# Kernel tuning notes

Measured on AMD Instinct MI355X. Metric: run time of the kernel, lower is better.

The kernel has to match this reference:

```python
import jax, jax.numpy as jnp
import numpy as np

N, D, N_CLASSES = 8192, 512, 128
POS_MARGIN = 1.0  # default path: sample_method=None, Dynamic_margin=None


def setup_inputs() -> dict:
    key = jax.random.key(0)
    k1, k2 = jax.random.split(key)
    x = jax.random.normal(k1, (N, D), dtype=jnp.float32)
    # metric-learning embeddings are L2-normalized so sim in [-1, 1]
    x = x / jnp.linalg.norm(x, axis=1, keepdims=True)
    targets = jax.random.randint(k2, (N,), 0, N_CLASSES, dtype=jnp.int64)
    return {"inputs": x, "targets": targets, "nonorm": 0}


def reference(inputs, targets, nonorm):
    n = inputs.shape[0]
    sim = jnp.matmul(inputs, inputs.T)                      # [n, n]
    same = targets[:, None] == targets[None, :]             # [n, n]
    pos_mask = same & (sim < POS_MARGIN)                    # drops self-sim == 1
    neg_mask = ~same

    # per-row masked log-sum-exp (sort in original is irrelevant to the sums)
    pos_sum = jnp.sum(jnp.where(pos_mask, jnp.exp(1.0 - sim), 0.0), axis=1)
    neg_sum = jnp.sum(jnp.where(neg_mask, jnp.exp(sim), 0.0), axis=1)
    pos_loss = jnp.log(pos_sum)
    neg_loss = jnp.log(neg_sum)

    has_neg = jnp.any(neg_mask, axis=1)                     # rows w/o negs are skipped
    loss = jnp.sum(jnp.where(has_neg, pos_loss + neg_loss, 0.0)) / n
    prec = jnp.mean(1.0 - has_neg.astype(jnp.float32))      # fraction of skipped rows

    # torch code reports means of the LAST row's pos/neg pairs
    last_pos = pos_mask[-1]
    last_neg = neg_mask[-1]
    mean_pos_sim = jnp.sum(jnp.where(last_pos, sim[-1], 0.0)) / jnp.sum(last_pos)
    mean_neg_sim = jnp.sum(jnp.where(last_neg, sim[-1], 0.0)) / jnp.sum(last_neg)
    return loss, prec, mean_pos_sim, mean_neg_sim
```

## Files before the change

kernel.cpp:

```cpp
#include <hip/hip_runtime.h>
#include <math.h>

#define N_ 8192
#define D_ 512
#define NC_ 128
#define T_ 64

typedef __attribute__((ext_vector_type(8))) short bf16x8;
typedef __attribute__((ext_vector_type(4))) float f32x4;
typedef __attribute__((ext_vector_type(4))) unsigned short us4;

static __device__ __forceinline__ unsigned short f2bf(float f) {
    union { float f; unsigned u; } c; c.f = f;
    unsigned u = c.u;
    u += 0x7fffu + ((u >> 16) & 1u);
    return (unsigned short)(u >> 16);
}

__global__ __launch_bounds__(256) void k_convert(const float* __restrict__ x,
                                                 unsigned short* __restrict__ xb) {
    int i = (blockIdx.x * 256 + threadIdx.x);
    float4 v = reinterpret_cast<const float4*>(x)[i];
    us4 o = { f2bf(v.x), f2bf(v.y), f2bf(v.z), f2bf(v.w) };
    reinterpret_cast<us4*>(xb)[i] = o;
}

__global__ __launch_bounds__(256, 4) void k_main(const unsigned short* __restrict__ xb,
                                                 const int* __restrict__ tg,
                                                 float* __restrict__ bufP,
                                                 float* __restrict__ bufN) {
    __shared__ alignas(16) unsigned short As[128 * 64];
    __shared__ alignas(16) unsigned short Bs[128 * 64];
    __shared__ int rowT[128];

    const int tid  = threadIdx.x;
    const int w    = tid >> 6;
    const int lane = tid & 63;
    const int q    = lane >> 4;
    const int l15  = lane & 15;
    const int wrow = w >> 1;
    const int wcol = w & 1;

    int rem = blockIdx.x;
    int it = 0;
    while (rem >= (T_ - it)) { rem -= (T_ - it); it++; }
    const int jt = it + rem;
    const int row0 = it * 128;
    const int col0 = jt * 128;

    if (tid < 128) rowT[tid] = tg[row0 + tid];
    __syncthreads();

    int tR[4][4];
#pragma unroll
    for (int mi = 0; mi < 4; ++mi)
#pragma unroll
        for (int r = 0; r < 4; ++r)
            tR[mi][r] = rowT[wrow * 64 + mi * 16 + q * 4 + r];

    int tC[4];
#pragma unroll
    for (int ni = 0; ni < 4; ++ni)
        tC[ni] = tg[col0 + wcol * 64 + ni * 16 + l15];

    f32x4 acc[4][4];
#pragma unroll
    for (int mi = 0; mi < 4; ++mi)
#pragma unroll
        for (int ni = 0; ni < 4; ++ni)
            acc[mi][ni] = (f32x4){0.f, 0.f, 0.f, 0.f};

    for (int ks = 0; ks < 8; ++ks) {
        const int k0 = ks * 64;
        __syncthreads();
#pragma unroll
        for (int itr = 0; itr < 4; ++itr) {
            int gs = (itr * 4 + w) * 64 + lane;
            int r  = gs >> 3;
            int s  = gs & 7;
            int g  = s ^ (r & 7);
            const unsigned short* ga = xb + (size_t)(row0 + r) * D_ + k0 + g * 8;
            const unsigned short* gb = xb + (size_t)(col0 + r) * D_ + k0 + g * 8;
            __builtin_amdgcn_global_load_lds(
                (const __attribute__((address_space(1))) void*)ga,
                (__attribute__((address_space(3))) void*)(As + (itr * 4 + w) * 512),
                16, 0, 0);
            __builtin_amdgcn_global_load_lds(
                (const __attribute__((address_space(1))) void*)gb,
                (__attribute__((address_space(3))) void*)(Bs + (itr * 4 + w) * 512),
                16, 0, 0);
        }
        __syncthreads();

#pragma unroll
        for (int kc = 0; kc < 2; ++kc) {
            bf16x8 aF[4], bF[4];
#pragma unroll
            for (int mi = 0; mi < 4; ++mi) {
                int rA = wrow * 64 + mi * 16 + l15;
                int g  = kc * 4 + q;
                int s  = g ^ (rA & 7);
                aF[mi] = *reinterpret_cast<const bf16x8*>(As + rA * 64 + s * 8);
            }
#pragma unroll
            for (int ni = 0; ni < 4; ++ni) {
                int rB = wcol * 64 + ni * 16 + l15;
                int g  = kc * 4 + q;
                int s  = g ^ (rB & 7);
                bF[ni] = *reinterpret_cast<const bf16x8*>(Bs + rB * 64 + s * 8);
            }
#pragma unroll
            for (int mi = 0; mi < 4; ++mi)
#pragma unroll
                for (int ni = 0; ni < 4; ++ni)
                    acc[mi][ni] = __builtin_amdgcn_mfma_f32_16x16x32_bf16(
                        aF[mi], bF[ni], acc[mi][ni], 0, 0, 0);
        }
    }

    float ps[4][4], ns[4][4];
    float cps[4], cns[4];
#pragma unroll
    for (int mi = 0; mi < 4; ++mi)
#pragma unroll
        for (int r = 0; r < 4; ++r) { ps[mi][r] = 0.f; ns[mi][r] = 0.f; }
#pragma unroll
    for (int ni = 0; ni < 4; ++ni) { cps[ni] = 0.f; cns[ni] = 0.f; }

#pragma unroll
    for (int mi = 0; mi < 4; ++mi)
#pragma unroll
        for (int ni = 0; ni < 4; ++ni)
#pragma unroll
            for (int r = 0; r < 4; ++r) {
                float s = acc[mi][ni][r];
                bool same = (tR[mi][r] == tC[ni]);
                float e = __expf(same ? 1.0f - s : s);
                float pe = (same && (s < 1.0f)) ? e : 0.0f;
                float ne = same ? 0.0f : e;
                ps[mi][r] += pe; ns[mi][r] += ne;
                cps[ni]   += pe; cns[ni]   += ne;
            }

    __syncthreads();
    float* scr = (float*)As;

#pragma unroll
    for (int mi = 0; mi < 4; ++mi)
#pragma unroll
        for (int r = 0; r < 4; ++r) {
            float p = ps[mi][r];
            float n = ns[mi][r];
#pragma unroll
            for (int m = 1; m < 16; m <<= 1) {
                p += __shfl_xor(p, m, 64);
                n += __shfl_xor(n, m, 64);
            }
            if (l15 == 0) {
                int rloc = wrow * 64 + mi * 16 + q * 4 + r;
                scr[wcol * 128 + rloc]       = p;
                scr[256 + wcol * 128 + rloc] = n;
            }
        }

#pragma unroll
    for (int ni = 0; ni < 4; ++ni) {
        float p = cps[ni];
        float n = cns[ni];
        p += __shfl_xor(p, 16, 64); p += __shfl_xor(p, 32, 64);
        n += __shfl_xor(n, 16, 64); n += __shfl_xor(n, 32, 64);
        if (q == 0) {
            int cloc = wcol * 64 + ni * 16 + l15;
            scr[512 + wrow * 128 + cloc] = p;
            scr[768 + wrow * 128 + cloc] = n;
        }
    }
    __syncthreads();

    if (tid < 128) {
        int r = tid;
        size_t off = ((size_t)it * T_ + jt) * 128 + r;
        bufP[off] = scr[r]       + scr[128 + r];
        bufN[off] = scr[256 + r] + scr[384 + r];
    } else if (jt != it) {
        int c = tid - 128;
        size_t off = ((size_t)jt * T_ + it) * 128 + c;
        bufP[off] = scr[512 + c] + scr[640 + c];
        bufN[off] = scr[768 + c] + scr[896 + c];
    }
}

__global__ __launch_bounds__(256) void k_last(const float* __restrict__ x,
                                              double* __restrict__ sim_last) {
    int j    = (blockIdx.x * 256 + threadIdx.x) >> 6;
    int lane = threadIdx.x & 63;
    const float* xl = x + (size_t)(N_ - 1) * D_;
    const float* xj = x + (size_t)j * D_;
    double acc = 0.0;
#pragma unroll
    for (int it = 0; it < 8; ++it) {
        int k = it * 64 + lane;
        acc += (double)xl[k] * (double)xj[k];
    }
#pragma unroll
    for (int m = 32; m >= 1; m >>= 1) acc += __shfl_xor(acc, m, 64);
    if (lane == 0) sim_last[j] = acc;
}

__global__ __launch_bounds__(256) void k_reduce(const float* __restrict__ bufP,
                                                const float* __restrict__ bufN,
                                                float* __restrict__ psum,
                                                float* __restrict__ nsum) {
    int t    = blockIdx.x;
    int half = threadIdx.x >> 7;
    int r    = threadIdx.x & 127;
    const float* buf = half ? bufN : bufP;
    const float* base = buf + (size_t)t * T_ * 128 + r;
    float s = 0.f;
#pragma unroll
    for (int o = 0; o < T_; ++o) s += base[o * 128];
    if (half) nsum[t * 128 + r] = s;
    else      psum[t * 128 + r] = s;
}

__global__ __launch_bounds__(1024) void k_final(const float* __restrict__ psum,
                                                const float* __restrict__ nsum,
                                                const int* __restrict__ tg,
                                                const double* __restrict__ sim_last,
                                                float* __restrict__ out) {
    __shared__ int lh[NC_];
    __shared__ double sl[1024], sp[1024], sn[1024];
    __shared__ int    sk[1024], cp[1024], cn[1024];
    int tid = threadIdx.x;

    if (tid < NC_) lh[tid] = 0;
    __syncthreads();
    for (int i = tid; i < N_; i += 1024) atomicAdd(&lh[tg[i]], 1);
    __syncthreads();

    double part = 0.0;
    int skip = 0;
    for (int i = tid; i < N_; i += 1024) {
        if (lh[tg[i]] < N_) {
            part += (double)(logf(psum[i]) + logf(nsum[i]));
        } else {
            skip++;
        }
    }

    double pd = 0.0, nd = 0.0;
    int pc = 0, nc = 0;
    int tlast = tg[N_ - 1];
    for (int j = tid; j < N_; j += 1024) {
        double s = sim_last[j];
        if (tg[j] == tlast) {
            if (s < 1.0) { pd += s; pc++; }
        } else {
            nd += s; nc++;
        }
    }

    sl[tid] = part; sk[tid] = skip;
    sp[tid] = pd;   cp[tid] = pc;
    sn[tid] = nd;   cn[tid] = nc;
    __syncthreads();
    for (int s = 512; s >= 1; s >>= 1) {
        if (tid < s) {
            sl[tid] += sl[tid + s]; sk[tid] += sk[tid + s];
            sp[tid] += sp[tid + s]; cp[tid] += cp[tid + s];
            sn[tid] += sn[tid + s]; cn[tid] += cn[tid + s];
        }
        __syncthreads();
    }
    if (tid == 0) {
        out[0] = (float)(sl[0] / (double)N_);
        out[1] = (float)sk[0] / (float)N_;
        out[2] = (float)(sp[0] / (double)cp[0]);
        out[3] = (float)(sn[0] / (double)cn[0]);
    }
}

extern "C" void kernel_launch(void* const* d_in, const int* in_sizes, int n_in,
                              void* d_out, int out_size, void* d_ws, size_t ws_size,
                              hipStream_t stream) {
    const float* x  = (const float*)d_in[0];
    const int*   tg = (const int*)d_in[1];
    char* ws = (char*)d_ws;

    unsigned short* xb = (unsigned short*)ws;
    const size_t XB = (size_t)N_ * D_ * 2;
    float*  psum     = (float*)(ws + XB);
    float*  nsum     = (float*)(ws + XB + 32768);
    double* sim_last = (double*)(ws + XB + 65536);
    float*  bufP     = (float*)(ws + XB + 131072);
    float*  bufN     = (float*)(ws + XB + 131072 + 2097152);

    const int nblk_tri = T_ * (T_ + 1) / 2;

    hipLaunchKernelGGL(k_convert, dim3((N_ * D_) / (256 * 4)), dim3(256), 0, stream, x, xb);
    hipLaunchKernelGGL(k_main, dim3(nblk_tri), dim3(256), 0, stream, xb, tg, bufP, bufN);
    hipLaunchKernelGGL(k_last, dim3((N_ * 64) / 256), dim3(256), 0, stream, x, sim_last);
    hipLaunchKernelGGL(k_reduce, dim3(T_), dim3(256), 0, stream, bufP, bufN, psum, nsum);
    hipLaunchKernelGGL(k_final, dim3(1), dim3(1024), 0, stream,
                       psum, nsum, tg, sim_last, (float*)d_out);
}
```

Before: 165.3 us.

## Double-buffer GEMM LDS tiles, swizzle block order, and fuse post-processing kernels

The main similarity kernel now uses two LDS buffers and issues asynchronous global-to-LDS loads two K-steps ahead, with explicit waitcnt and barriers. This overlaps memory latency with MFMA work, and setprio raises priority during the MFMA burst. Block indices are swizzled across the triangular tile grid, and occupancy is lowered to 2 blocks per CU to fit the doubled shared memory. The separate last-row, reduce and final kernels are merged into one 64-block post kernel that finishes through global atomics and a last-block-done counter, cutting launches and removing the single-block tail, at the cost of atomic ordering subtleties.

```diff
diff --git a/kernel.cpp b/kernel.cpp
--- a/kernel.cpp
+++ b/kernel.cpp
@@ -5,6 +5,8 @@
 #define D_ 512
 #define NC_ 128
 #define T_ 64
+#define BK_ 64
+#define KSTEPS 8
 
 typedef __attribute__((ext_vector_type(8))) short bf16x8;
 typedef __attribute__((ext_vector_type(4))) float f32x4;
@@ -17,21 +19,31 @@
     return (unsigned short)(u >> 16);
 }
 
-__global__ __launch_bounds__(256) void k_convert(const float* __restrict__ x,
-                                                 unsigned short* __restrict__ xb) {
-    int i = (blockIdx.x * 256 + threadIdx.x);
+__global__ __launch_bounds__(256) void k_pre(const float* __restrict__ x,
+                                             unsigned short* __restrict__ xb,
+                                             double* __restrict__ gd,
+                                             int* __restrict__ gi) {
+    const int bid = blockIdx.x;
+    const int tid = threadIdx.x;
+    if (bid == 0 && tid == 0) {
+        atomicExch((unsigned long long*)&gd[0], 0ull);
+        atomicExch((unsigned long long*)&gd[1], 0ull);
+        atomicExch((unsigned long long*)&gd[2], 0ull);
+        atomicExch(&gi[0], 0); atomicExch(&gi[1], 0);
+        atomicExch(&gi[2], 0); atomicExch(&gi[3], 0);
+    }
+    int i = bid * 256 + tid;
     float4 v = reinterpret_cast<const float4*>(x)[i];
     us4 o = { f2bf(v.x), f2bf(v.y), f2bf(v.z), f2bf(v.w) };
     reinterpret_cast<us4*>(xb)[i] = o;
 }
 
-__global__ __launch_bounds__(256, 4) void k_main(const unsigned short* __restrict__ xb,
+__global__ __launch_bounds__(256, 2) void k_main(const unsigned short* __restrict__ xb,
                                                  const int* __restrict__ tg,
                                                  float* __restrict__ bufP,
                                                  float* __restrict__ bufN) {
-    __shared__ alignas(16) unsigned short As[128 * 64];
-    __shared__ alignas(16) unsigned short Bs[128 * 64];
-    __shared__ int rowT[128];
+    __shared__ alignas(16) unsigned short As[2][128 * 64];
+    __shared__ alignas(16) unsigned short Bs[2][128 * 64];
 
     const int tid  = threadIdx.x;
     const int w    = tid >> 6;
@@ -41,38 +53,17 @@
     const int wrow = w >> 1;
     const int wcol = w & 1;
 
-    int rem = blockIdx.x;
+    const int bswz = (blockIdx.x & 7) * 260 + (blockIdx.x >> 3);
+
+    int rem = bswz;
     int it = 0;
     while (rem >= (T_ - it)) { rem -= (T_ - it); it++; }
     const int jt = it + rem;
     const int row0 = it * 128;
     const int col0 = jt * 128;
 
-    if (tid < 128) rowT[tid] = tg[row0 + tid];
-    __syncthreads();
-
-    int tR[4][4];
-#pragma unroll
-    for (int mi = 0; mi < 4; ++mi)
-#pragma unroll
-        for (int r = 0; r < 4; ++r)
-            tR[mi][r] = rowT[wrow * 64 + mi * 16 + q * 4 + r];
-
-    int tC[4];
-#pragma unroll
-    for (int ni = 0; ni < 4; ++ni)
-        tC[ni] = tg[col0 + wcol * 64 + ni * 16 + l15];
-
-    f32x4 acc[4][4];
-#pragma unroll
-    for (int mi = 0; mi < 4; ++mi)
-#pragma unroll
-        for (int ni = 0; ni < 4; ++ni)
-            acc[mi][ni] = (f32x4){0.f, 0.f, 0.f, 0.f};
-
-    for (int ks = 0; ks < 8; ++ks) {
-        const int k0 = ks * 64;
-        __syncthreads();
+    auto stage_tile = [&](int p, int kt) {
+        const int k0 = kt * BK_;
 #pragma unroll
         for (int itr = 0; itr < 4; ++itr) {
             int gs = (itr * 4 + w) * 64 + lane;
@@ -83,47 +74,90 @@
             const unsigned short* gb = xb + (size_t)(col0 + r) * D_ + k0 + g * 8;
             __builtin_amdgcn_global_load_lds(
                 (const __attribute__((address_space(1))) void*)ga,
-                (__attribute__((address_space(3))) void*)(As + (itr * 4 + w) * 512),
+                (__attribute__((address_space(3))) void*)(&As[p][0] + (itr * 4 + w) * 512),
                 16, 0, 0);
             __builtin_amdgcn_global_load_lds(
                 (const __attribute__((address_space(1))) void*)gb,
-                (__attribute__((address_space(3))) void*)(Bs + (itr * 4 + w) * 512),
+                (__attribute__((address_space(3))) void*)(&Bs[p][0] + (itr * 4 + w) * 512),
                 16, 0, 0);
         }
-        __syncthreads();
-
+    };
+
+    f32x4 acc[4][4];
+#pragma unroll
+    for (int mi = 0; mi < 4; ++mi)
+#pragma unroll
+        for (int ni = 0; ni < 4; ++ni)
+            acc[mi][ni] = (f32x4){0.f, 0.f, 0.f, 0.f};
+
+    auto compute_tile = [&](int p) {
 #pragma unroll
         for (int kc = 0; kc < 2; ++kc) {
             bf16x8 aF[4], bF[4];
 #pragma unroll
             for (int mi = 0; mi < 4; ++mi) {
                 int rA = wrow * 64 + mi * 16 + l15;
-                int g  = kc * 4 + q;
-                int s  = g ^ (rA & 7);
-                aF[mi] = *reinterpret_cast<const bf16x8*>(As + rA * 64 + s * 8);
+                int sl = (kc * 4 + q) ^ (rA & 7);
+                aF[mi] = *reinterpret_cast<const bf16x8*>(&As[p][0] + rA * 64 + sl * 8);
             }
 #pragma unroll
             for (int ni = 0; ni < 4; ++ni) {
                 int rB = wcol * 64 + ni * 16 + l15;
-                int g  = kc * 4 + q;
-                int s  = g ^ (rB & 7);
-                bF[ni] = *reinterpret_cast<const bf16x8*>(Bs + rB * 64 + s * 8);
-            }
+                int sl = (kc * 4 + q) ^ (rB & 7);
+                bF[ni] = *reinterpret_cast<const bf16x8*>(&Bs[p][0] + rB * 64 + sl * 8);
+            }
+            asm volatile("s_waitcnt lgkmcnt(0)" ::: "memory");
+            __builtin_amdgcn_sched_barrier(0);
+            __builtin_amdgcn_s_setprio(1);
 #pragma unroll
             for (int mi = 0; mi < 4; ++mi)
 #pragma unroll
                 for (int ni = 0; ni < 4; ++ni)
                     acc[mi][ni] = __builtin_amdgcn_mfma_f32_16x16x32_bf16(
                         aF[mi], bF[ni], acc[mi][ni], 0, 0, 0);
-        }
-    }
+            __builtin_amdgcn_s_setprio(0);
+        }
+    };
+
+#define TILE(P, KS, DOSTAGE, VMN)                                         \
+    do {                                                                  \
+        asm volatile("s_waitcnt vmcnt(" #VMN ")" ::: "memory");           \
+        __builtin_amdgcn_s_barrier();                                     \
+        __builtin_amdgcn_sched_barrier(0);                                \
+        compute_tile(P);                                                  \
+        __builtin_amdgcn_s_barrier();                                     \
+        __builtin_amdgcn_sched_barrier(0);                                \
+        if (DOSTAGE) stage_tile(P, (KS) + 2);                             \
+    } while (0)
+
+    stage_tile(0, 0);
+    stage_tile(1, 1);
+
+    TILE(0, 0, 1, 8);
+    TILE(1, 1, 1, 8);
+    TILE(0, 2, 1, 8);
+    TILE(1, 3, 1, 8);
+    TILE(0, 4, 1, 8);
+    TILE(1, 5, 1, 8);
+    TILE(0, 6, 0, 8);
+    TILE(1, 7, 0, 0);
+#undef TILE
+
+    int tC[4];
+#pragma unroll
+    for (int ni = 0; ni < 4; ++ni)
+        tC[ni] = tg[col0 + wcol * 64 + ni * 16 + l15];
 
     float ps[4][4], ns[4][4];
     float cps[4], cns[4];
+    int tR[4][4];
 #pragma unroll
     for (int mi = 0; mi < 4; ++mi)
 #pragma unroll
-        for (int r = 0; r < 4; ++r) { ps[mi][r] = 0.f; ns[mi][r] = 0.f; }
+        for (int r = 0; r < 4; ++r) {
+            ps[mi][r] = 0.f; ns[mi][r] = 0.f;
+            tR[mi][r] = tg[row0 + wrow * 64 + mi * 16 + q * 4 + r];
+        }
 #pragma unroll
     for (int ni = 0; ni < 4; ++ni) { cps[ni] = 0.f; cns[ni] = 0.f; }
 
@@ -142,9 +176,7 @@
                 cps[ni]   += pe; cns[ni]   += ne;
             }
 
-    __syncthreads();
     float* scr = (float*)As;
-
 #pragma unroll
     for (int mi = 0; mi < 4; ++mi)
 #pragma unroll
@@ -190,93 +222,101 @@
     }
 }
 
-__global__ __launch_bounds__(256) void k_last(const float* __restrict__ x,
-                                              double* __restrict__ sim_last) {
-    int j    = (blockIdx.x * 256 + threadIdx.x) >> 6;
-    int lane = threadIdx.x & 63;
-    const float* xl = x + (size_t)(N_ - 1) * D_;
-    const float* xj = x + (size_t)j * D_;
-    double acc = 0.0;
-#pragma unroll
-    for (int it = 0; it < 8; ++it) {
-        int k = it * 64 + lane;
-        acc += (double)xl[k] * (double)xj[k];
-    }
-#pragma unroll
-    for (int m = 32; m >= 1; m >>= 1) acc += __shfl_xor(acc, m, 64);
-    if (lane == 0) sim_last[j] = acc;
-}
-
-__global__ __launch_bounds__(256) void k_reduce(const float* __restrict__ bufP,
-                                                const float* __restrict__ bufN,
-                                                float* __restrict__ psum,
-                                                float* __restrict__ nsum) {
-    int t    = blockIdx.x;
-    int half = threadIdx.x >> 7;
-    int r    = threadIdx.x & 127;
-    const float* buf = half ? bufN : bufP;
+__global__ __launch_bounds__(256) void k_post(const float* __restrict__ bufP,
+                                              const float* __restrict__ bufN,
+                                              const int* __restrict__ tg,
+                                              const float* __restrict__ x,
+                                              double* __restrict__ gd,
+                                              int* __restrict__ gi,
+                                              float* __restrict__ out) {
+    __shared__ int lh[NC_];
+    __shared__ float sv[256];
+    __shared__ double Rd[256], Pd[256], Nd[256];
+    __shared__ int Ri[256], Pc[256], Nc[256];
+    const int t   = blockIdx.x;
+    const int tid = threadIdx.x;
+
+    if (tid < NC_) lh[tid] = 0;
+    __syncthreads();
+#pragma unroll
+    for (int i = 0; i < 32; ++i) atomicAdd(&lh[tg[i * 256 + tid]], 1);
+    __syncthreads();
+
+    const int half = tid >> 7;
+    const int r    = tid & 127;
+    const float* buf  = half ? bufN : bufP;
     const float* base = buf + (size_t)t * T_ * 128 + r;
     float s = 0.f;
 #pragma unroll
     for (int o = 0; o < T_; ++o) s += base[o * 128];
-    if (half) nsum[t * 128 + r] = s;
-    else      psum[t * 128 + r] = s;
-}
-
-__global__ __launch_bounds__(1024) void k_final(const float* __restrict__ psum,
-                                                const float* __restrict__ nsum,
-                                                const int* __restrict__ tg,
-                                                const double* __restrict__ sim_last,
-                                                float* __restrict__ out) {
-    __shared__ int lh[NC_];
-    __shared__ double sl[1024], sp[1024], sn[1024];
-    __shared__ int    sk[1024], cp[1024], cn[1024];
-    int tid = threadIdx.x;
-
-    if (tid < NC_) lh[tid] = 0;
-    __syncthreads();
-    for (int i = tid; i < N_; i += 1024) atomicAdd(&lh[tg[i]], 1);
-    __syncthreads();
-
-    double part = 0.0;
-    int skip = 0;
-    for (int i = tid; i < N_; i += 1024) {
-        if (lh[tg[i]] < N_) {
-            part += (double)(logf(psum[i]) + logf(nsum[i]));
-        } else {
-            skip++;
-        }
-    }
-
+    sv[tid] = s;
+    __syncthreads();
+
+    double rd = 0.0; int ri = 0;
+    if (tid < 128) {
+        int row = t * 128 + tid;
+        bool ok = lh[tg[row]] < N_;
+        rd = ok ? (double)(logf(sv[tid]) + logf(sv[128 + tid])) : 0.0;
+        ri = ok ? 0 : 1;
+    }
+
+    const int wv   = tid >> 6;
+    const int lane = tid & 63;
+    const int tlast = tg[N_ - 1];
+    const float* xl = x + (size_t)(N_ - 1) * D_;
     double pd = 0.0, nd = 0.0;
     int pc = 0, nc = 0;
-    int tlast = tg[N_ - 1];
-    for (int j = tid; j < N_; j += 1024) {
-        double s = sim_last[j];
-        if (tg[j] == tlast) {
-            if (s < 1.0) { pd += s; pc++; }
-        } else {
-            nd += s; nc++;
-        }
-    }
-
-    sl[tid] = part; sk[tid] = skip;
-    sp[tid] = pd;   cp[tid] = pc;
-    sn[tid] = nd;   cn[tid] = nc;
-    __syncthreads();
-    for (int s = 512; s >= 1; s >>= 1) {
-        if (tid < s) {
-            sl[tid] += sl[tid + s]; sk[tid] += sk[tid + s];
-            sp[tid] += sp[tid + s]; cp[tid] += cp[tid + s];
-            sn[tid] += sn[tid + s]; cn[tid] += cn[tid + s];
+    for (int rep = 0; rep < 32; ++rep) {
+        int row = t * 128 + rep * 4 + wv;
+        const float* xj = x + (size_t)row * D_;
+        double acc = 0.0;
+#pragma unroll
+        for (int itk = 0; itk < 8; ++itk) {
+            int k = itk * 64 + lane;
+            acc += (double)xl[k] * (double)xj[k];
+        }
+#pragma unroll
+        for (int m = 32; m >= 1; m >>= 1) acc += __shfl_xor(acc, m, 64);
+        if (lane == 0) {
+            int tgr = tg[row];
+            if (tgr == tlast) { if (acc < 1.0) { pd += acc; pc++; } }
+            else              { nd += acc; nc++; }
+        }
+    }
+
+    Rd[tid] = rd; Ri[tid] = ri;
+    Pd[tid] = pd; Pc[tid] = pc;
+    Nd[tid] = nd; Nc[tid] = nc;
+    __syncthreads();
+    for (int st = 128; st >= 1; st >>= 1) {
+        if (tid < st) {
+            Rd[tid] += Rd[tid + st]; Pd[tid] += Pd[tid + st]; Nd[tid] += Nd[tid + st];
+            Ri[tid] += Ri[tid + st]; Pc[tid] += Pc[tid + st]; Nc[tid] += Nc[tid + st];
         }
         __syncthreads();
     }
+
     if (tid == 0) {
-        out[0] = (float)(sl[0] / (double)N_);
-        out[1] = (float)sk[0] / (float)N_;
-        out[2] = (float)(sp[0] / (double)cp[0]);
-        out[3] = (float)(sn[0] / (double)cn[0]);
+        atomicAdd(&gd[0], Rd[0]);
+        atomicAdd(&gd[1], Pd[0]);
+        atomicAdd(&gd[2], Nd[0]);
+        atomicAdd(&gi[0], Ri[0]);
+        atomicAdd(&gi[1], Pc[0]);
+        atomicAdd(&gi[2], Nc[0]);
+        __threadfence();
+        int old = atomicAdd(&gi[3], 1);
+        if ((old & 63) == 63) {
+            double A = atomicAdd(&gd[0], 0.0);
+            double B = atomicAdd(&gd[1], 0.0);
+            double C = atomicAdd(&gd[2], 0.0);
+            int U = atomicAdd(&gi[0], 0);
+            int V = atomicAdd(&gi[1], 0);
+            int Y = atomicAdd(&gi[2], 0);
+            out[0] = (float)(A / (double)N_);
+            out[1] = (float)U / (float)N_;
+            out[2] = (float)(B / (double)V);
+            out[3] = (float)(C / (double)Y);
+        }
     }
 }
 
@@ -289,18 +329,16 @@
 
     unsigned short* xb = (unsigned short*)ws;
     const size_t XB = (size_t)N_ * D_ * 2;
-    float*  psum     = (float*)(ws + XB);
-    float*  nsum     = (float*)(ws + XB + 32768);
-    double* sim_last = (double*)(ws + XB + 65536);
-    float*  bufP     = (float*)(ws + XB + 131072);
-    float*  bufN     = (float*)(ws + XB + 131072 + 2097152);
+    float*  bufP = (float*)(ws + XB);
+    float*  bufN = (float*)(ws + XB + 2097152);
+    double* gd   = (double*)(ws + XB + 4194304);
+    int*    gi   = (int*)(ws + XB + 4194304 + 64);
 
     const int nblk_tri = T_ * (T_ + 1) / 2;
 
-    hipLaunchKernelGGL(k_convert, dim3((N_ * D_) / (256 * 4)), dim3(256), 0, stream, x, xb);
+    hipLaunchKernelGGL(k_pre, dim3((N_ * D_) / (256 * 4)), dim3(256), 0, stream,
+                       x, xb, gd, gi);
     hipLaunchKernelGGL(k_main, dim3(nblk_tri), dim3(256), 0, stream, xb, tg, bufP, bufN);
-    hipLaunchKernelGGL(k_last, dim3((N_ * 64) / 256), dim3(256), 0, stream, x, sim_last);
-    hipLaunchKernelGGL(k_reduce, dim3(T_), dim3(256), 0, stream, bufP, bufN, psum, nsum);
-    hipLaunchKernelGGL(k_final, dim3(1), dim3(1024), 0, stream,
-                       psum, nsum, tg, sim_last, (float*)d_out);
-}
+    hipLaunchKernelGGL(k_post, dim3(T_), dim3(256), 0, stream,
+                       bufP, bufN, tg, x, gd, gi, (float*)d_out);
+}
```

Result: no change. 166.9 us (+1.0%).
